# Kernel optimization log

Hardware: AMD Instinct MI355X
Metric: run time of the kernel (lower is better)

Reference implementation:

```python
import jax, jax.numpy as jnp
import numpy as np

# Standard SMPL kinematic tree (parent of joint i); root parent = -1 (unused)
PARENTS = [-1, 0, 0, 0, 1, 2, 3, 4, 5, 6, 7, 8, 9, 9, 9, 12, 13, 14, 16, 17, 18, 19, 20, 21]
NUM_JOINTS = 24
NUM_VERTS = 6890
BATCH = 1024


def rodrigues(aa):
    """Axis-angle [..., 3] -> rotation matrices [..., 3, 3] (Rodrigues formula)."""
    eps = 1e-8
    theta = jnp.sqrt(jnp.sum(aa * aa, axis=-1, keepdims=True) + eps)  # [...,1]
    axis = aa / theta
    c = jnp.cos(theta)[..., None]
    s = jnp.sin(theta)[..., None]
    kx, ky, kz = axis[..., 0], axis[..., 1], axis[..., 2]
    zero = jnp.zeros_like(kx)
    K = jnp.stack([zero, -kz, ky, kz, zero, -kx, -ky, kx, zero], axis=-1)
    K = K.reshape(aa.shape[:-1] + (3, 3))
    I = jnp.eye(3, dtype=aa.dtype)
    return I + s * K + (1.0 - c) * (K @ K)


def make44(R, t):
    """R: [B,3,3], t: [B,3] -> homogeneous transform [B,4,4] (th_with_zeros)."""
    B = R.shape[0]
    top = jnp.concatenate([R, t[:, :, None]], axis=2)  # [B,3,4]
    bottom = jnp.broadcast_to(jnp.array([0.0, 0.0, 0.0, 1.0], dtype=R.dtype), (B, 1, 4))
    return jnp.concatenate([top, bottom], axis=1)


def setup_inputs() -> dict:
    key = jax.random.key(0)
    ks = jax.random.split(key, 8)
    return {
        "th_pose_axisang": jax.random.normal(ks[0], (BATCH, NUM_JOINTS * 3), dtype=jnp.float32),
        "th_betas": jax.random.normal(ks[1], (BATCH, 10), dtype=jnp.float32),
        "th_trans": jax.random.normal(ks[2], (BATCH, 3), dtype=jnp.float32),
        "v_template": jax.random.normal(ks[3], (NUM_VERTS, 3), dtype=jnp.float32),
        "shapedirs": jax.random.normal(ks[4], (NUM_VERTS, 3, 10), dtype=jnp.float32),
        "posedirs": jax.random.normal(ks[5], (NUM_VERTS, 3, 207), dtype=jnp.float32),
        "J_regressor": jax.random.uniform(ks[6], (NUM_JOINTS, NUM_VERTS), dtype=jnp.float32),
        "weights": jax.random.uniform(ks[7], (NUM_VERTS, NUM_JOINTS), dtype=jnp.float32),
    }


def reference(th_pose_axisang, th_betas, th_trans, v_template, shapedirs, posedirs, J_regressor, weights):
    B = th_pose_axisang.shape[0]
    dt = th_pose_axisang.dtype

    # pose map: all joint rotmats; non-root rotmats minus identity (subtract_flat_id)
    rots = rodrigues(th_pose_axisang.reshape(B, NUM_JOINTS, 3))  # [B,24,3,3]
    pose_map = (rots[:, 1:] - jnp.eye(3, dtype=dt)).reshape(B, (NUM_JOINTS - 1) * 9)  # [B,207]

    v_shaped = v_template[None] + jnp.einsum('vcs,bs->bvc', shapedirs, th_betas)   # [B,V,3]
    th_j = jnp.einsum('jv,bvc->bjc', J_regressor, v_shaped)                        # [B,24,3]
    v_posed = v_shaped + jnp.einsum('vcp,bp->bvc', posedirs, pose_map)             # [B,V,3]

    # forward kinematics along the fixed 24-joint chain
    results = [make44(rots[:, 0], th_j[:, 0])]
    for i in range(1, NUM_JOINTS):
        p = PARENTS[i]
        rel = make44(rots[:, i], th_j[:, i] - th_j[:, p])
        results.append(results[p] @ rel)
    G = jnp.stack(results, axis=1)  # [B,24,4,4] global transforms

    # remove rest-pose joint location from translation column (th_pack subtraction)
    j_h = jnp.concatenate([th_j, jnp.zeros((B, NUM_JOINTS, 1), dtype=dt)], axis=-1)  # [B,24,4]
    t_corr = jnp.einsum('bjmn,bjn->bjm', G, j_h)                                      # [B,24,4]
    G2 = jnp.concatenate([G[..., :3], (G[..., 3] - t_corr)[..., None]], axis=-1)      # [B,24,4,4]

    # linear blend skinning: per-vertex blended transform applied to rest shape
    T = jnp.einsum('bjmn,vj->bvmn', G2, weights)  # [B,V,4,4] (== th_T reordered)
    rest_h = jnp.concatenate([v_posed, jnp.ones((B, NUM_VERTS, 1), dtype=dt)], axis=-1)  # [B,V,4]
    th_verts = jnp.einsum('bvmn,bvn->bvm', T, rest_h)[..., :3]  # [B,V,3]

    th_jtr = G[:, :, :3, 3]  # [B,24,3]

    # th_trans is nonzero -> translation branch
    th_verts = th_verts + th_trans[:, None]
    th_jtr = th_jtr + th_trans[:, None]
    return th_verts, th_jtr
```

## Files before the change

### kernel.cpp

```cpp
#include <hip/hip_runtime.h>
#include <hip/hip_bf16.h>

#define NJ 24
#define NV 6890
#define NB 1024
#define V3 (NV*3)
#define JTR_OFF (NB*NV*3)

typedef __attribute__((ext_vector_type(8))) short bf16x8;
typedef __attribute__((ext_vector_type(4))) float f32x4;
typedef float f4u __attribute__((ext_vector_type(4), aligned(4)));

__constant__ int c_par[NJ] = {-1,0,0,0,1,2,3,4,5,6,7,8,9,9,9,12,13,14,16,17,18,19,20,21};

__global__ void k0(const float* __restrict__ Jreg, const float* __restrict__ vtempl,
                   const float* __restrict__ shdirs, float* __restrict__ Jc)
{
    int j = blockIdx.x;
    float acc[33];
#pragma unroll
    for (int i = 0; i < 33; ++i) acc[i] = 0.0f;

    for (int v = blockIdx.y * 256 + threadIdx.x; v < NV; v += 1024) {
        float r = Jreg[j * NV + v];
#pragma unroll
        for (int c = 0; c < 3; ++c) {
            acc[c * 11 + 10] += r * vtempl[v * 3 + c];
            const float* sd = &shdirs[(v * 3 + c) * 10];
#pragma unroll
            for (int s = 0; s < 10; ++s) acc[c * 11 + s] += r * sd[s];
        }
    }
#pragma unroll
    for (int i = 0; i < 33; ++i) {
        float x = acc[i];
        for (int o = 32; o > 0; o >>= 1) x += __shfl_down(x, o, 64);
        acc[i] = x;
    }
    __shared__ float red[4][33];
    int w = threadIdx.x >> 6, l = threadIdx.x & 63;
    if (l == 0) {
#pragma unroll
        for (int i = 0; i < 33; ++i) red[w][i] = acc[i];
    }
    __syncthreads();
    if (threadIdx.x < 33) {
        float s = red[0][threadIdx.x] + red[1][threadIdx.x] +
                  red[2][threadIdx.x] + red[3][threadIdx.x];
        atomicAdd(&Jc[j * 33 + threadIdx.x], s);
    }
}

__global__ void kpack(const float* __restrict__ pdirs, const float* __restrict__ shdirs,
                      const float* __restrict__ vtempl, __hip_bfloat16* __restrict__ pdBsw)
{
    int cid = blockIdx.x * 256 + threadIdx.x;
    int v64 = cid & 63;
    int t = cid >> 6;
    int kq = t & 3; t >>= 2;
    int c = t % 3; t /= 3;
    int kt = t % 7;
    int vt = t / 7;
    int v = vt * 64 + v64;

    ushort tmp[8] __attribute__((aligned(16)));
#pragma unroll
    for (int j = 0; j < 8; ++j) {
        int k = kt * 32 + kq * 8 + j;
        float val = 0.0f;
        if (v < NV) {
            if (k < 207)       val = pdirs[(v * 3 + c) * 207 + k];
            else if (k < 217)  val = shdirs[(v * 3 + c) * 10 + (k - 207)];
            else if (k == 217) val = vtempl[v * 3 + c];
        }
        __hip_bfloat16 h = __float2bfloat16(val);
        tmp[j] = *(ushort*)&h;
    }
    ((float4*)pdBsw)[cid] = *(const float4*)tmp;
}

__global__ void kwB(const float* __restrict__ wts, __hip_bfloat16* __restrict__ wtsB)
{
    int t = blockIdx.x * 256 + threadIdx.x;
    int v64 = t & 63;
    int kq = (t >> 6) & 3;
    int vt = t >> 8;
    int v = vt * 64 + v64;

    ushort tmp[8] __attribute__((aligned(16)));
#pragma unroll
    for (int j8 = 0; j8 < 8; ++j8) {
        int j = kq * 8 + j8;
        float val = (v < NV && j < NJ) ? wts[v * NJ + j] : 0.0f;
        __hip_bfloat16 h = __float2bfloat16(val);
        tmp[j8] = *(ushort*)&h;
    }
    ((float4*)wtsB)[t] = *(const float4*)tmp;
}

__device__ __forceinline__ void writeA(__hip_bfloat16* ABsw, int b, int k, float val)
{
    int btile = b >> 6, b6 = b & 63, kt = k >> 5, kq = (k >> 3) & 3, j = k & 7;
    __hip_bfloat16 h = __float2bfloat16(val);
    ABsw[((((btile * 7) + kt) * 4 + kq) * 64 + b6) * 8 + j] = h;
}

__global__ void k1(const float* __restrict__ pose, const float* __restrict__ betas,
                   const float* __restrict__ trans, const float* __restrict__ Jc,
                   __hip_bfloat16* __restrict__ ABsw, __hip_bfloat16* __restrict__ G2B,
                   float* __restrict__ out)
{
    __shared__ float rots[4][NJ][9];
    __shared__ float thj [4][NJ][3];
    __shared__ float res [4][NJ][16];

    int w = threadIdx.x >> 6;
    int l = threadIdx.x & 63;
    int b = blockIdx.x * 4 + w;

    if (l < NJ) {
        int j = l;
        float ax = pose[b * 72 + j * 3 + 0];
        float ay = pose[b * 72 + j * 3 + 1];
        float az = pose[b * 72 + j * 3 + 2];
        float theta = sqrtf(ax * ax + ay * ay + az * az + 1e-8f);
        float inv = 1.0f / theta;
        float kx = ax * inv, ky = ay * inv, kz = az * inv;
        float c = cosf(theta), s = sinf(theta), mc = 1.0f - c;
        float R[9];
        R[0] = 1.0f - mc * (ky * ky + kz * kz);
        R[1] = -s * kz + mc * (kx * ky);
        R[2] =  s * ky + mc * (kx * kz);
        R[3] =  s * kz + mc * (kx * ky);
        R[4] = 1.0f - mc * (kx * kx + kz * kz);
        R[5] = -s * kx + mc * (ky * kz);
        R[6] = -s * ky + mc * (kx * kz);
        R[7] =  s * kx + mc * (ky * kz);
        R[8] = 1.0f - mc * (kx * kx + ky * ky);
#pragma unroll
        for (int e = 0; e < 9; ++e) rots[w][j][e] = R[e];
        if (j >= 1) {
            int base = (j - 1) * 9;
#pragma unroll
            for (int e = 0; e < 9; ++e) {
                float val = R[e] - ((e == 0 || e == 4 || e == 8) ? 1.0f : 0.0f);
                writeA(ABsw, b, base + e, val);
            }
        }
#pragma unroll
        for (int c3 = 0; c3 < 3; ++c3) {
            float acc = Jc[(j * 3 + c3) * 11 + 10];
#pragma unroll
            for (int s10 = 0; s10 < 10; ++s10)
                acc += Jc[(j * 3 + c3) * 11 + s10] * betas[b * 10 + s10];
            thj[w][j][c3] = acc;
        }
    } else if (l < 41) {
        int k = 207 + (l - 24);
        float val;
        if (l < 34)       val = betas[b * 10 + (l - 24)];
        else if (l == 34) val = 1.0f;
        else              val = 0.0f;
        writeA(ABsw, b, k, val);
    }
    __syncthreads();

    if (l < 16) {
        int m = l >> 2, n = l & 3;
        float v;
        if (m < 3) v = (n < 3) ? rots[w][0][m * 3 + n] : thj[w][0][m];
        else       v = (n == 3) ? 1.0f : 0.0f;
        res[w][0][l] = v;
    }
    __syncthreads();
#pragma unroll
    for (int i = 1; i < NJ; ++i) {
        int p = c_par[i];
        if (l < 16) {
            int m = l >> 2, n = l & 3;
            float acc = 0.0f;
#pragma unroll
            for (int k3 = 0; k3 < 3; ++k3) {
                float relkn = (n < 3) ? rots[w][i][k3 * 3 + n]
                                      : (thj[w][i][k3] - thj[w][p][k3]);
                acc += res[w][p][m * 4 + k3] * relkn;
            }
            if (n == 3) acc += res[w][p][m * 4 + 3];
            res[w][i][l] = acc;
        }
        __syncthreads();
    }

    if (l < NJ) {
        int j = l;
#pragma unroll
        for (int c3 = 0; c3 < 3; ++c3)
            out[JTR_OFF + b * 72 + j * 3 + c3] = res[w][j][c3 * 4 + 3] + trans[b * 3 + c3];
    }
    for (int k = l; k < 384; k += 64) {
        int mc = k >> 5, j = k & 31;
        int m = mc >> 2, n = mc & 3;
        float v = 0.0f;
        if (j < NJ) {
            if (n < 3) v = res[w][j][m * 4 + n];
            else v = res[w][j][m * 4 + 3] - (res[w][j][m * 4 + 0] * thj[w][j][0] +
                                             res[w][j][m * 4 + 1] * thj[w][j][1] +
                                             res[w][j][m * 4 + 2] * thj[w][j][2]);
        }
        __hip_bfloat16 h = __float2bfloat16(v);
        G2B[mc * 32768 + ((((b >> 6) * 4) + (j >> 3)) * 64 + (b & 63)) * 8 + (j & 7)] = h;
    }
}

__launch_bounds__(256, 3)
__global__ void k2g(const __hip_bfloat16* __restrict__ pdBsw,
                    const __hip_bfloat16* __restrict__ ABsw,
                    const __hip_bfloat16* __restrict__ G2B,
                    const __hip_bfloat16* __restrict__ wtsB,
                    const float* __restrict__ trans,
                    float* __restrict__ outp)
{
    __shared__ __align__(16) char smem[32 * 204 * 4];
    ushort* As = (ushort*)smem;
    ushort* Bs = (ushort*)(smem + 12288);
    float*  outs = (float*)smem;

    int tid = threadIdx.x;
    int wgid = blockIdx.y * 108 + blockIdx.x;
    int lin  = (wgid & 7) * 216 + (wgid >> 3);
    int vtile = lin >> 4;
    int btile = lin & 15;
    int wid = tid >> 6, lane = tid & 63;
    int waveb = wid & 1, wavev = wid >> 1;
    int kq = lane >> 4, l15 = lane & 15;

    const float4* pA4 = (const float4*)pdBsw;
    const float4* pB4 = (const float4*)ABsw;

    f32x4 acc[3][2][2] = {};

    int aoff = (kq * 64 + waveb * 32 + l15) * 8;
    int boff = (kq * 64 + wavev * 32 + l15) * 8;

    for (int kt = 0; kt < 7; ++kt) {
        int abase = (vtile * 7 + kt) * 768;
        int bbase = (btile * 7 + kt) * 256;
        ((float4*)As)[tid]       = pA4[abase + tid];
        ((float4*)As)[tid + 256] = pA4[abase + tid + 256];
        ((float4*)As)[tid + 512] = pA4[abase + tid + 512];
        ((float4*)Bs)[tid]       = pB4[bbase + tid];
        __syncthreads();

        bf16x8 af[2];
#pragma unroll
        for (int mi = 0; mi < 2; ++mi)
            af[mi] = *(const bf16x8*)&Bs[aoff + mi * 128];
#pragma unroll
        for (int c = 0; c < 3; ++c) {
            bf16x8 bfr[2];
#pragma unroll
            for (int ni = 0; ni < 2; ++ni)
                bfr[ni] = *(const bf16x8*)&As[boff + c * 2048 + ni * 128];
#pragma unroll
            for (int mi = 0; mi < 2; ++mi)
#pragma unroll
                for (int ni = 0; ni < 2; ++ni)
                    acc[c][mi][ni] = __builtin_amdgcn_mfma_f32_16x16x32_bf16(
                        af[mi], bfr[ni], acc[c][mi][ni], 0, 0, 0);
        }
        __syncthreads();
    }

    bf16x8 wf[2];
#pragma unroll
    for (int ni = 0; ni < 2; ++ni)
        wf[ni] = *(const bf16x8*)&wtsB[(((vtile * 4 + kq) * 64) +
                                        wavev * 32 + ni * 16 + l15) * 8];

    int bframe = ((btile * 4 + kq) * 64 + waveb * 32 + l15) * 8;

    float res3[2][2][4][3];
#pragma unroll
    for (int mi = 0; mi < 2; ++mi) {
#pragma unroll
        for (int m = 0; m < 3; ++m) {
            f32x4 T[4][2] = {};
#pragma unroll
            for (int c4 = 0; c4 < 4; ++c4) {
                int mc = m * 4 + c4;
                bf16x8 gf = *(const bf16x8*)&G2B[mc * 32768 + bframe + mi * 128];
#pragma unroll
                for (int ni = 0; ni < 2; ++ni)
                    T[c4][ni] = __builtin_amdgcn_mfma_f32_16x16x32_bf16(
                        gf, wf[ni], T[c4][ni], 0, 0, 0);
            }
#pragma unroll
            for (int ni = 0; ni < 2; ++ni) {
#pragma unroll
                for (int r = 0; r < 4; ++r) {
                    int bl = waveb * 32 + mi * 16 + (kq << 2) + r;
                    int b  = btile * 64 + bl;
                    float x = acc[0][mi][ni][r];
                    float y = acc[1][mi][ni][r];
                    float z = acc[2][mi][ni][r];
                    res3[mi][ni][r][m] = T[3][ni][r] + T[0][ni][r] * x +
                                         T[1][ni][r] * y + T[2][ni][r] * z +
                                         trans[b * 3 + m];
                }
            }
        }
    }

    int fvalid = (NV - vtile * 64) * 3;
    if (fvalid > 192) fvalid = 192;
#pragma unroll
    for (int pass = 0; pass < 2; ++pass) {
        if (waveb == pass) {
#pragma unroll
            for (int mi = 0; mi < 2; ++mi) {
#pragma unroll
                for (int ni = 0; ni < 2; ++ni) {
                    int vl = wavev * 32 + ni * 16 + l15;
#pragma unroll
                    for (int r = 0; r < 4; ++r) {
                        int row = mi * 16 + (kq << 2) + r;
#pragma unroll
                        for (int m = 0; m < 3; ++m)
                            outs[row * 204 + vl * 3 + m] = res3[mi][ni][r][m];
                    }
                }
            }
        }
        __syncthreads();
        if (lane < 48) {
            int fbase = lane * 4;
#pragma unroll
            for (int it = 0; it < 8; ++it) {
                int bl = wid * 8 + it;
                int b  = btile * 64 + pass * 32 + bl;
                const float* src = &outs[bl * 204 + fbase];
                float* dst = &outp[(size_t)b * V3 + (size_t)vtile * 192 + fbase];
                if (fbase + 4 <= fvalid) {
                    *(f4u*)dst = *(const f4u*)src;
                } else {
#pragma unroll
                    for (int k2 = 0; k2 < 4; ++k2)
                        if (fbase + k2 < fvalid) dst[k2] = src[k2];
                }
            }
        }
        if (pass == 0) __syncthreads();
    }
}

extern "C" void kernel_launch(void* const* d_in, const int* in_sizes, int n_in,
                              void* d_out, int out_size, void* d_ws, size_t ws_size,
                              hipStream_t stream)
{
    const float* pose   = (const float*)d_in[0];
    const float* betas  = (const float*)d_in[1];
    const float* trans  = (const float*)d_in[2];
    const float* vtempl = (const float*)d_in[3];
    const float* shdirs = (const float*)d_in[4];
    const float* pdirs  = (const float*)d_in[5];
    const float* Jreg   = (const float*)d_in[6];
    const float* wts    = (const float*)d_in[7];
    float* out = (float*)d_out;
    char* ws = (char*)d_ws;

    float* Jc              = (float*)(ws);
    __hip_bfloat16* ABsw   = (__hip_bfloat16*)(ws + 4096);
    __hip_bfloat16* G2B    = (__hip_bfloat16*)(ws + 462848);
    __hip_bfloat16* wtsB   = (__hip_bfloat16*)(ws + 1249280);
    __hip_bfloat16* pdBsw  = (__hip_bfloat16*)(ws + 1691648);

    hipMemsetAsync(Jc, 0, NJ * 33 * sizeof(float), stream);
    hipLaunchKernelGGL(k0, dim3(NJ, 4), dim3(256), 0, stream, Jreg, vtempl, shdirs, Jc);
    hipLaunchKernelGGL(kpack, dim3(2268), dim3(256), 0, stream, pdirs, shdirs, vtempl, pdBsw);
    hipLaunchKernelGGL(kwB, dim3(108), dim3(256), 0, stream, wts, wtsB);
    hipLaunchKernelGGL(k1, dim3(NB / 4), dim3(256), 0, stream,
                       pose, betas, trans, Jc, ABsw, G2B, out);
    hipLaunchKernelGGL(k2g, dim3(108, 16), dim3(256), 0, stream,
                       pdBsw, ABsw, G2B, wtsB, trans, out);
}
```

Baseline: 186.1 us.

## Double-buffer k2g GEMM tiles via direct global-to-LDS async loads

Replaces the register-staged global→LDS copies in the k2g main loop with global_load_lds direct-to-LDS transfers into two ping-pong buffers. The next K tile is prefetched while the current one is consumed, with vmcnt waits and raw barriers in place of __syncthreads. The aim is to hide global load latency behind the MFMA work and cut register traffic. Shared memory rises to 32 KB, which may lower occupancy, and the hand-written waitcnt sequencing is fragile.

```diff
diff --git a/kernel.cpp b/kernel.cpp
--- a/kernel.cpp
+++ b/kernel.cpp
@@ -212,6 +212,13 @@
     }
 }
 
+__device__ __forceinline__ void gld16(const void* g, void* l)
+{
+    __builtin_amdgcn_global_load_lds(
+        (const __attribute__((address_space(1))) void*)g,
+        (__attribute__((address_space(3))) void*)l, 16, 0, 0);
+}
+
 __launch_bounds__(256, 3)
 __global__ void k2g(const __hip_bfloat16* __restrict__ pdBsw,
                     const __hip_bfloat16* __restrict__ ABsw,
@@ -220,10 +227,8 @@
                     const float* __restrict__ trans,
                     float* __restrict__ outp)
 {
-    __shared__ __align__(16) char smem[32 * 204 * 4];
-    ushort* As = (ushort*)smem;
-    ushort* Bs = (ushort*)(smem + 12288);
-    float*  outs = (float*)smem;
+    __shared__ __align__(16) char smem[2 * 16384];
+    float* outs = (float*)smem;
 
     int tid = threadIdx.x;
     int wgid = blockIdx.y * 108 + blockIdx.x;
@@ -234,22 +239,34 @@
     int waveb = wid & 1, wavev = wid >> 1;
     int kq = lane >> 4, l15 = lane & 15;
 
-    const float4* pA4 = (const float4*)pdBsw;
-    const float4* pB4 = (const float4*)ABsw;
+    auto stage = [&](int kb, int kt) {
+        char* dst = smem + kb * 16384;
+        const ushort* gA = (const ushort*)pdBsw + (size_t)(vtile * 7 + kt) * 6144;
+        const ushort* gB = (const ushort*)ABsw  + (size_t)(btile * 7 + kt) * 2048;
+#pragma unroll
+        for (int i = 0; i < 3; ++i)
+            gld16(gA + (i * 256 + wid * 64 + lane) * 8, dst + i * 4096 + wid * 1024);
+        gld16(gB + (wid * 64 + lane) * 8, dst + 12288 + wid * 1024);
+    };
 
     f32x4 acc[3][2][2] = {};
 
     int aoff = (kq * 64 + waveb * 32 + l15) * 8;
     int boff = (kq * 64 + wavev * 32 + l15) * 8;
 
+    stage(0, 0);
     for (int kt = 0; kt < 7; ++kt) {
-        int abase = (vtile * 7 + kt) * 768;
-        int bbase = (btile * 7 + kt) * 256;
-        ((float4*)As)[tid]       = pA4[abase + tid];
-        ((float4*)As)[tid + 256] = pA4[abase + tid + 256];
-        ((float4*)As)[tid + 512] = pA4[abase + tid + 512];
-        ((float4*)Bs)[tid]       = pB4[bbase + tid];
-        __syncthreads();
+        if (kt < 6) {
+            stage((kt + 1) & 1, kt + 1);
+            asm volatile("s_waitcnt vmcnt(4)" ::: "memory");
+        } else {
+            asm volatile("s_waitcnt vmcnt(0)" ::: "memory");
+        }
+        __builtin_amdgcn_s_barrier();
+        asm volatile("" ::: "memory");
+
+        const ushort* As = (const ushort*)(smem + (kt & 1) * 16384);
+        const ushort* Bs = As + 6144;
 
         bf16x8 af[2];
 #pragma unroll
@@ -268,7 +285,8 @@
                     acc[c][mi][ni] = __builtin_amdgcn_mfma_f32_16x16x32_bf16(
                         af[mi], bfr[ni], acc[c][mi][ni], 0, 0, 0);
         }
-        __syncthreads();
+        __builtin_amdgcn_s_barrier();
+        asm volatile("" ::: "memory");
     }
 
     bf16x8 wf[2];
```

New measurement: 186.4 us. Within noise of the previous version (+0.1%).
